# Optimization experiments

Measured on AMD Instinct MI355X. Metric: run time of the kernel, lower is better.

## Reference

```python
import jax, jax.numpy as jnp
import numpy as np

E = 1024   # embed_dim
H = 16     # num_heads
D = E // H # head_dim = 64
HD2 = D // 2
B = 2
S = 2048


def setup_inputs() -> dict:
    key = jax.random.key(0)
    ks = jax.random.split(key, 12)
    def lin(k, fan_in, fan_out):
        # xavier-uniform-ish init, stored in [in, out] (jax) convention
        lim = float(np.sqrt(6.0 / (fan_in + fan_out)))
        return jax.random.uniform(k, (fan_in, fan_out), jnp.float32, -lim, lim)
    return {
        "query": jax.random.normal(ks[0], (B, S, E), jnp.float32),
        "xi_scale": jax.random.uniform(ks[1], (B,), jnp.float32),
        "Wq": lin(ks[2], E, E), "bq": jnp.zeros((E,), jnp.float32),
        "Wk": lin(ks[3], E, E), "bk": jnp.zeros((E,), jnp.float32),
        "Wv": lin(ks[4], E, E), "bv": jnp.zeros((E,), jnp.float32),
        "Wo": lin(ks[5], E, E), "bo": jnp.zeros((E,), jnp.float32),
        "enc_w1": lin(ks[6], 1, HD2), "enc_b1": jnp.zeros((HD2,), jnp.float32),
        "ln_g": jnp.ones((HD2,), jnp.float32), "ln_b": jnp.zeros((HD2,), jnp.float32),
        "enc_w2": lin(ks[7], HD2, D), "enc_b2": jnp.zeros((D,), jnp.float32),
        "scale_gating": jnp.ones((H,), jnp.float32),
    }


def reference(query, xi_scale, Wq, bq, Wk, bk, Wv, bv, Wo, bo,
              enc_w1, enc_b1, ln_g, ln_b, enc_w2, enc_b2, scale_gating):
    b, s, e = query.shape
    h, d = H, e // H
    # --- scale adaptation: xi -> Linear -> LayerNorm -> GELU -> Linear ---
    x = xi_scale[:, None] @ enc_w1 + enc_b1                  # [B, D/2]
    mu = x.mean(-1, keepdims=True)
    var = ((x - mu) ** 2).mean(-1, keepdims=True)
    x = (x - mu) / jnp.sqrt(var + 1e-5) * ln_g + ln_b
    x = jax.nn.gelu(x, approximate=False)
    xe = x @ enc_w2 + enc_b2                                 # [B, D]
    adapt = 1.0 + jax.nn.sigmoid(scale_gating)[None, :, None] * xe[:, None, :]  # [B, H, D]
    # --- projections (self-attention: key = value = query) ---
    q = (query @ Wq + bq).reshape(b, s, h, d).transpose(0, 2, 1, 3) * adapt[:, :, None, :]
    k = (query @ Wk + bk).reshape(b, s, h, d).transpose(0, 2, 1, 3) * adapt[:, :, None, :]
    v = (query @ Wv + bv).reshape(b, s, h, d).transpose(0, 2, 1, 3)
    # --- explicit QK^T / sqrt(d) -> softmax -> V ---
    inv_scale = 1.0 / float(np.sqrt(d))
    scores = jnp.einsum('bhqd,bhkd->bhqk', q, k) * inv_scale  # [B, H, S, S]
    attn = jax.nn.softmax(scores, axis=-1)
    out = jnp.einsum('bhqk,bhkd->bhqd', attn, v)              # [B, H, S, D]
    out = out.transpose(0, 2, 1, 3).reshape(b, s, e)
    return out @ Wo + bo
```

## Files before the change

### kernel.cpp

```cpp
#include <hip/hip_runtime.h>

typedef __bf16 bf16;
typedef __attribute__((ext_vector_type(8))) __bf16 bf16x8;
typedef __attribute__((ext_vector_type(4))) float f32x4;
typedef __attribute__((ext_vector_type(16))) float f32x16;
typedef unsigned int u32;

#define MFMA16(a, b, c) __builtin_amdgcn_mfma_f32_16x16x32_bf16((a), (b), (c), 0, 0, 0)
#define MFMA32(a, b, c) __builtin_amdgcn_mfma_f32_32x32x16_bf16((a), (b), (c), 0, 0, 0)

#define BB 2
#define SS 2048
#define EE 1024
#define HH 16
#define DD 64
#define MM (BB * SS)

__device__ inline f32x4 zero4() {
    f32x4 z; z.x = 0.f; z.y = 0.f; z.z = 0.f; z.w = 0.f; return z;
}

__device__ __forceinline__ void gload16(const bf16* g, bf16* l) {
    __builtin_amdgcn_global_load_lds(
        (const __attribute__((address_space(1))) u32*)(const void*)g,
        (__attribute__((address_space(3))) u32*)(void*)l,
        16, 0, 0);
}

__device__ __forceinline__ u32 pkbf(float a, float b) {
    union { __bf16 h; unsigned short s; } ua, ub;
    ua.h = (__bf16)a; ub.h = (__bf16)b;
    return (u32)ua.s | ((u32)ub.s << 16);
}

__global__ __launch_bounds__(256) void prep_kernel(
    const float* __restrict__ query, bf16* __restrict__ qc,
    const float* __restrict__ s0, const float* __restrict__ s1,
    const float* __restrict__ s2, const float* __restrict__ s3,
    bf16* __restrict__ d0, bf16* __restrict__ d1,
    bf16* __restrict__ d2, bf16* __restrict__ d3,
    const float* __restrict__ xi, const float* __restrict__ w1,
    const float* __restrict__ b1, const float* __restrict__ lng,
    const float* __restrict__ lnb, const float* __restrict__ w2,
    const float* __restrict__ b2, const float* __restrict__ gate,
    float* __restrict__ adapt) {
    __shared__ bf16 tile[64 * 72];
    const int bid = blockIdx.x;
    const int t = threadIdx.x;

    if (bid < 2048) {
        const int i = (bid * 256 + t) * 8;
        float4 a = *(const float4*)(query + i);
        float4 b = *(const float4*)(query + i + 4);
        bf16 tmp[8];
        tmp[0] = (bf16)a.x; tmp[1] = (bf16)a.y; tmp[2] = (bf16)a.z; tmp[3] = (bf16)a.w;
        tmp[4] = (bf16)b.x; tmp[5] = (bf16)b.y; tmp[6] = (bf16)b.z; tmp[7] = (bf16)b.w;
        *(uint4*)(qc + i) = *(uint4*)tmp;
    } else if (bid < 3072) {
        const int m = (bid - 2048) >> 8;
        const int idx0 = (bid - 2048) & 255;
        const float* W = (m == 0) ? s0 : (m == 1) ? s1 : (m == 2) ? s2 : s3;
        bf16* Wt = (m == 0) ? d0 : (m == 1) ? d1 : (m == 2) ? d2 : d3;
        const int k0 = (idx0 >> 4) * 64, n0 = (idx0 & 15) * 64;
#pragma unroll
        for (int i = 0; i < 2; ++i) {
            int idx = i * 256 + t;
            int r = idx >> 3, c = (idx & 7) * 8;
            float4 a = *(const float4*)(W + (k0 + r) * EE + n0 + c);
            float4 b = *(const float4*)(W + (k0 + r) * EE + n0 + c + 4);
            bf16 tmp[8];
            tmp[0] = (bf16)a.x; tmp[1] = (bf16)a.y; tmp[2] = (bf16)a.z; tmp[3] = (bf16)a.w;
            tmp[4] = (bf16)b.x; tmp[5] = (bf16)b.y; tmp[6] = (bf16)b.z; tmp[7] = (bf16)b.w;
            *(uint4*)(tile + r * 72 + c) = *(uint4*)tmp;
        }
        __syncthreads();
#pragma unroll
        for (int i = 0; i < 2; ++i) {
            int idx = i * 256 + t;
            int n = idx >> 3, kc = (idx & 7) * 8;
            bf16 tmp[8];
#pragma unroll
            for (int j = 0; j < 8; ++j) tmp[j] = tile[(kc + j) * 72 + n];
            *(uint4*)(Wt + (n0 + n) * EE + k0 + kc) = *(uint4*)tmp;
        }
    } else {
        const int b = bid - 3072;
        float* xs = (float*)tile;
        if (t < 64) {
            const float xiv = xi[b];
            float xv = 0.f;
            if (t < 32) xv = xiv * w1[t] + b1[t];
            float sm = xv;
            for (int off = 1; off < 32; off <<= 1) sm += __shfl_xor(sm, off);
            const float mu = sm * (1.f / 32.f);
            float dv = (t < 32) ? (xv - mu) : 0.f;
            float s2 = dv * dv;
            for (int off = 1; off < 32; off <<= 1) s2 += __shfl_xor(s2, off);
            const float var = s2 * (1.f / 32.f);
            if (t < 32) {
                float xn = (xv - mu) * rsqrtf(var + 1e-5f) * lng[t] + lnb[t];
                float ge = 0.5f * xn * (1.f + erff(xn * 0.70710678118654752f));
                xs[t] = ge;
            }
        }
        __syncthreads();
        if (t < 64) {
            float acc = b2[t];
            for (int j = 0; j < 32; ++j) acc += xs[j] * w2[j * DD + t];
            for (int h = 0; h < HH; ++h) {
                float sg = 1.f / (1.f + __expf(-gate[h]));
                adapt[(b * HH + h) * DD + t] = 1.f + sg * acc;
            }
        }
    }
}

__global__ __launch_bounds__(256, 3) void gemm_qkv(
    const bf16* __restrict__ Aq, const bf16* __restrict__ Bqk,
    const bf16* __restrict__ Av,
    const float* __restrict__ bias, const float* __restrict__ bias2,
    const float* __restrict__ bias3, const float* __restrict__ adapt,
    bf16* __restrict__ outqk, bf16* __restrict__ outvt) {
    __shared__ bf16 As[2 * 128 * 32];
    __shared__ bf16 Bs[2 * 128 * 32];

    const int t = threadIdx.x;
    const int w = t >> 6, lane = t & 63;
    const int mrow = lane & 15, quad = lane >> 4;
    const int wm = (w & 1) * 64, wn = (w >> 1) * 64;

    int md, bx, by;
    const bf16 *Ap, *Bp;
    int bid = blockIdx.x;
    if (bid < 512) { md = 5; bx = bid & 31; by = bid >> 5; Ap = Aq; Bp = Bqk; }
    else { md = 4; bid -= 512; bx = bid & 7; by = bid >> 3; Ap = Av; Bp = Aq; }
    const int m0 = bx * 128, n0 = by * 128;

    f32x4 acc[4][4];
#pragma unroll
    for (int i = 0; i < 4; ++i)
#pragma unroll
        for (int j = 0; j < 4; ++j) acc[i][j] = zero4();

    const int dr = lane >> 2;
    const int dcg = ((lane & 3) ^ (dr & 3)) * 8;
    const bf16* Ag = Ap + (size_t)(m0 + w * 16 + dr) * EE + dcg;
    const bf16* Bg = Bp + (size_t)(n0 + w * 16 + dr) * EE + dcg;
    bf16* Al = As + (w * 16) * 32;
    bf16* Bl = Bs + (w * 16) * 32;

    gload16(Ag, Al);
    gload16(Ag + 64 * EE, Al + 64 * 32);
    gload16(Bg, Bl);
    gload16(Bg + 64 * EE, Bl + 64 * 32);

    for (int kt = 0; kt < 32; ++kt) {
        __syncthreads();
        if (kt < 31) {
            const int kn = (kt + 1) * 32;
            const int nb = (kt + 1) & 1;
            gload16(Ag + kn, Al + nb * 4096);
            gload16(Ag + 64 * EE + kn, Al + nb * 4096 + 64 * 32);
            gload16(Bg + kn, Bl + nb * 4096);
            gload16(Bg + 64 * EE + kn, Bl + nb * 4096 + 64 * 32);
        }
        const bf16* Ab = As + (kt & 1) * 4096;
        const bf16* Bb = Bs + (kt & 1) * 4096;
        const int sw = (quad ^ (mrow & 3)) * 8;
        bf16x8 af[4], bfr[4];
#pragma unroll
        for (int i = 0; i < 4; ++i)
            af[i] = *(const bf16x8*)(Ab + (wm + i * 16 + mrow) * 32 + sw);
#pragma unroll
        for (int j = 0; j < 4; ++j)
            bfr[j] = *(const bf16x8*)(Bb + (wn + j * 16 + mrow) * 32 + sw);
#pragma unroll
        for (int i = 0; i < 4; ++i)
#pragma unroll
            for (int j = 0; j < 4; ++j)
                acc[i][j] = MFMA16(af[i], bfr[j], acc[i][j]);
    }

#pragma unroll
    for (int i = 0; i < 4; ++i) {
#pragma unroll
        for (int j = 0; j < 4; ++j) {
            const int col = n0 + wn + j * 16 + mrow;
#pragma unroll
            for (int r = 0; r < 4; ++r) {
                const int row = m0 + wm + i * 16 + quad * 4 + r;
                float v = acc[i][j][r];
                if (md == 4) {
                    v += bias3[row];
                    const int h = row >> 6, d = row & 63;
                    const int b = col >> 11, s = col & (SS - 1);
                    outvt[(((b * HH + h) * DD + d) * SS) + s] = (bf16)v;
                } else {
                    const int m2 = col >> 10;
                    const int cl = col & 1023;
                    const int h = cl >> 6, d = cl & 63;
                    const int b = row >> 11, s = row & (SS - 1);
                    v += (m2 ? bias2[cl] : bias[cl]);
                    v *= adapt[(b * HH + h) * DD + d];
                    if (!m2) v *= 0.18033688011113811f;
                    outqk[(size_t)m2 * MM * EE + ((b * HH + h) * SS + s) * DD + d] = (bf16)v;
                }
            }
        }
    }
}

__global__ __launch_bounds__(256, 3) void gemm_o(
    const bf16* __restrict__ A, const bf16* __restrict__ Bt,
    const float* __restrict__ bias, float* __restrict__ outf) {
    __shared__ bf16 As[2 * 128 * 64];
    __shared__ bf16 Bs[2 * 64 * 64];

    const int t = threadIdx.x;
    const int w = t >> 6, lane = t & 63;
    const int mrow = lane & 15, quad = lane >> 4;
    const int m0 = blockIdx.x * 128, n0 = blockIdx.y * 64;

    f32x4 acc[2][4];
#pragma unroll
    for (int i = 0; i < 2; ++i)
#pragma unroll
        for (int j = 0; j < 4; ++j) acc[i][j] = zero4();

    const int grow = lane >> 3;
    const int gsw = ((lane & 7) ^ grow) * 8;
    const bf16* Ag = A + (size_t)(m0 + w * 32 + grow) * EE + gsw;
    const bf16* Bg = Bt + (size_t)(n0 + w * 16 + grow) * EE + gsw;
    bf16* Al = As + (w * 32) * 64;
    bf16* Bl = Bs + (w * 16) * 64;

#pragma unroll
    for (int i = 0; i < 4; ++i) gload16(Ag + i * 8 * EE, Al + i * 8 * 64);
#pragma unroll
    for (int i = 0; i < 2; ++i) gload16(Bg + i * 8 * EE, Bl + i * 8 * 64);

    for (int kt = 0; kt < 16; ++kt) {
        __syncthreads();
        if (kt < 15) {
            const int kn = (kt + 1) * 64;
            const int nb = (kt + 1) & 1;
#pragma unroll
            for (int i = 0; i < 4; ++i)
                gload16(Ag + i * 8 * EE + kn, Al + nb * 8192 + i * 8 * 64);
#pragma unroll
            for (int i = 0; i < 2; ++i)
                gload16(Bg + i * 8 * EE + kn, Bl + nb * 4096 + i * 8 * 64);
        }
        const bf16* Ab = As + (kt & 1) * 8192;
        const bf16* Bb = Bs + (kt & 1) * 4096;
#pragma unroll
        for (int ks = 0; ks < 2; ++ks) {
            const int cg = ks * 4 + quad;
            const int sw = (cg ^ (mrow & 7)) * 8;
            bf16x8 af[2], bfr[4];
#pragma unroll
            for (int mi = 0; mi < 2; ++mi)
                af[mi] = *(const bf16x8*)(Ab + (w * 32 + mi * 16 + mrow) * 64 + sw);
#pragma unroll
            for (int nj = 0; nj < 4; ++nj)
                bfr[nj] = *(const bf16x8*)(Bb + (nj * 16 + mrow) * 64 + sw);
#pragma unroll
            for (int mi = 0; mi < 2; ++mi)
#pragma unroll
                for (int nj = 0; nj < 4; ++nj)
                    acc[mi][nj] = MFMA16(af[mi], bfr[nj], acc[mi][nj]);
        }
    }

#pragma unroll
    for (int mi = 0; mi < 2; ++mi) {
#pragma unroll
        for (int nj = 0; nj < 4; ++nj) {
            const int col = n0 + nj * 16 + mrow;
#pragma unroll
            for (int r = 0; r < 4; ++r) {
                const int row = m0 + w * 32 + mi * 16 + quad * 4 + r;
                outf[row * EE + col] = acc[mi][nj][r] + bias[col];
            }
        }
    }
}

__global__ __launch_bounds__(256, 2) void attn_kernel(
    const bf16* __restrict__ q, const bf16* __restrict__ k,
    const bf16* __restrict__ vt, bf16* __restrict__ o0) {
    __shared__ bf16 lds[16384];
    bf16* Ks = lds;
    bf16* Vs = lds + 8192;

    const int t = threadIdx.x;
    const int w = t >> 6, lane = t & 63;
    const int q32 = lane & 31, h = lane >> 5;
    const int bh = blockIdx.x & 31;
    const int qb = blockIdx.x >> 5;
    const int qr0 = qb * 128 + w * 32;

    bf16x8 qf[4];
#pragma unroll
    for (int c = 0; c < 4; ++c)
        qf[c] = *(const bf16x8*)(q + (size_t)(bh * SS + qr0 + q32) * DD + c * 16 + h * 8);

    f32x16 oacc[2];
#pragma unroll
    for (int mf = 0; mf < 2; ++mf)
#pragma unroll
        for (int i = 0; i < 16; ++i) oacc[mf][i] = 0.f;
    float lsum = 0.f;

    const int dr = lane >> 3;
    const int dcg = ((lane & 7) ^ dr) * 8;
    const bf16* kg = k + (size_t)bh * SS * DD;
    const bf16* vg = vt + (size_t)bh * DD * SS;
    const bf16* kgl = kg + (size_t)dr * DD + dcg;
    const bf16* vgl = vg + (size_t)(w * 16 + dr) * SS + dcg;

#pragma unroll
    for (int i = 0; i < 2; ++i) {
        const int rb = w * 16 + i * 8;
        gload16(kgl + (size_t)rb * DD, Ks + rb * 64);
        gload16(vgl + (size_t)(i * 8) * SS, Vs + rb * 64);
    }

    for (int kt = 0; kt < SS / 64; ++kt) {
        __syncthreads();
        if (kt < SS / 64 - 1) {
            const int nb = (kt + 1) & 1;
#pragma unroll
            for (int i = 0; i < 2; ++i) {
                const int rb = w * 16 + i * 8;
                gload16(kgl + (size_t)((kt + 1) * 64 + rb) * DD, Ks + nb * 4096 + rb * 64);
                gload16(vgl + (size_t)(i * 8) * SS + (kt + 1) * 64, Vs + nb * 4096 + rb * 64);
            }
        }
        const bf16* Kb = Ks + (kt & 1) * 4096;
        const bf16* Vb = Vs + (kt & 1) * 4096;

        f32x16 st[2];
#pragma unroll
        for (int mf = 0; mf < 2; ++mf)
#pragma unroll
            for (int i = 0; i < 16; ++i) st[mf][i] = 0.f;
#pragma unroll
        for (int c = 0; c < 4; ++c) {
            const int sw = ((2 * c + h) ^ (q32 & 7)) * 8;
#pragma unroll
            for (int mf = 0; mf < 2; ++mf) {
                bf16x8 kf = *(const bf16x8*)(Kb + (mf * 32 + q32) * 64 + sw);
                st[mf] = MFMA32(kf, qf[c], st[mf]);
            }
        }

        u32 P32[2][8];
#pragma unroll
        for (int mf = 0; mf < 2; ++mf)
#pragma unroll
            for (int rp = 0; rp < 8; ++rp) {
                float pa = __builtin_amdgcn_exp2f(st[mf][2 * rp]);
                float pb = __builtin_amdgcn_exp2f(st[mf][2 * rp + 1]);
                lsum += pa + pb;
                P32[mf][rp] = pkbf(pa, pb);
            }

#pragma unroll
        for (int c = 0; c < 4; ++c) {
            const int mfs = c >> 1;
            const int ro = (c & 1) * 4;
            union { u32 u[4]; bf16x8 v; } pb;
            {
                u32 vA0 = P32[mfs][ro + 0], vA1 = P32[mfs][ro + 1];
                u32 vB0 = P32[mfs][ro + 2], vB1 = P32[mfs][ro + 3];
                u32 prep0 = h ? vA0 : vB0;
                u32 prep1 = h ? vA1 : vB1;
                u32 sh0 = __shfl_xor(prep0, 32);
                u32 sh1 = __shfl_xor(prep1, 32);
                pb.u[0] = h ? sh0 : vA0;
                pb.u[1] = h ? sh1 : vA1;
                pb.u[2] = h ? vB0 : sh0;
                pb.u[3] = h ? vB1 : sh1;
            }
            const int sw = ((2 * c + h) ^ (q32 & 7)) * 8;
#pragma unroll
            for (int mf = 0; mf < 2; ++mf) {
                bf16x8 vf = *(const bf16x8*)(Vb + (mf * 32 + q32) * 64 + sw);
                oacc[mf] = MFMA32(vf, pb.v, oacc[mf]);
            }
        }
    }

    lsum += __shfl_xor(lsum, 32);
    const float inv = 1.f / lsum;

    __syncthreads();
    bf16* ob = lds + w * 2112;
#pragma unroll
    for (int mf = 0; mf < 2; ++mf)
#pragma unroll
        for (int rp = 0; rp < 8; ++rp) {
            const int d = 32 * mf + 2 * (rp & 1) + 8 * (rp >> 1) + 4 * h;
            *(u32*)(ob + q32 * 66 + d) =
                pkbf(oacc[mf][2 * rp] * inv, oacc[mf][2 * rp + 1] * inv);
        }
    __syncthreads();

    const int b = bh >> 4, head = bh & 15;
    const int half = lane & 1;
    const int r = lane >> 1;
#pragma unroll
    for (int i = 0; i < 4; ++i) {
        bf16x8 val = *(const bf16x8*)(ob + r * 66 + half * 32 + i * 8);
        *(bf16x8*)(o0 + (size_t)(b * SS + qr0 + r) * EE + head * DD +
                   half * 32 + i * 8) = val;
    }
}

extern "C" void kernel_launch(void* const* d_in, const int* in_sizes, int n_in,
                              void* d_out, int out_size, void* d_ws, size_t ws_size,
                              hipStream_t stream) {
    const float* query = (const float*)d_in[0];
    const float* xi    = (const float*)d_in[1];
    const float* Wq = (const float*)d_in[2];  const float* bq = (const float*)d_in[3];
    const float* Wk = (const float*)d_in[4];  const float* bk = (const float*)d_in[5];
    const float* Wv = (const float*)d_in[6];  const float* bv = (const float*)d_in[7];
    const float* Wo = (const float*)d_in[8];  const float* bo = (const float*)d_in[9];
    const float* ew1 = (const float*)d_in[10]; const float* eb1 = (const float*)d_in[11];
    const float* lng = (const float*)d_in[12]; const float* lnb = (const float*)d_in[13];
    const float* ew2 = (const float*)d_in[14]; const float* eb2 = (const float*)d_in[15];
    const float* gate = (const float*)d_in[16];
    float* out = (float*)d_out;

    char* ws = (char*)d_ws;
    const size_t SZ = (size_t)MM * EE * sizeof(bf16);
    const size_t WSZ = (size_t)EE * EE * sizeof(bf16);

    bf16* queryc = (bf16*)(ws);
    bf16* p0     = (bf16*)(ws);
    bf16* qws    = (bf16*)(ws + SZ);
    bf16* kws    = (bf16*)(ws + 2 * SZ);
    bf16* vtws   = (bf16*)(ws + 3 * SZ);
    bf16* wqT    = (bf16*)(ws + 4 * SZ);
    bf16* wkT    = (bf16*)(ws + 4 * SZ + WSZ);
    bf16* wvT    = (bf16*)(ws + 4 * SZ + 2 * WSZ);
    bf16* woT    = (bf16*)(ws + 4 * SZ + 3 * WSZ);
    float* adaptws = (float*)(ws + 4 * SZ + 4 * WSZ);

    prep_kernel<<<3074, 256, 0, stream>>>(query, queryc, Wq, Wk, Wv, Wo,
                                          wqT, wkT, wvT, woT,
                                          xi, ew1, eb1, lng, lnb, ew2, eb2, gate,
                                          adaptws);

    gemm_qkv<<<768, 256, 0, stream>>>(queryc, wqT, wvT, bq, bk, bv, adaptws,
                                      qws, vtws);

    attn_kernel<<<512, 256, 0, stream>>>(qws, kws, vtws, p0);

    gemm_o<<<dim3(MM / 128, EE / 64), 256, 0, stream>>>(p0, woT, bo, out);
}
```

Baseline: 217.1 us.

## Store K and V in MFMA fragment order and load attention operands directly from global

The QKV projection epilogue now writes K and V^T in a pre-swizzled layout that matches the per-lane MFMA fragment order. The attention kernel drops the LDS double-buffered staging and its per-tile barriers, loading K and V fragments straight from global or L2 into registers, with K prefetched one tile ahead and MFMA sections given raised wave priority. This removes LDS traffic and synchronisation but leaves each wave exposed to global load latency, raises register pressure, and has every wave re-read the same K/V from cache.

```diff
diff --git a/kernel.cpp b/kernel.cpp
--- a/kernel.cpp
+++ b/kernel.cpp
@@ -194,7 +194,12 @@
                     v += bias3[row];
                     const int h = row >> 6, d = row & 63;
                     const int b = col >> 11, s = col & (SS - 1);
-                    outvt[(((b * HH + h) * DD + d) * SS) + s] = (bf16)v;
+                    const int bh = b * HH + h;
+                    const int kt2 = s >> 6, ci = (s >> 4) & 3, ji = s & 7;
+                    const int mfi = (d >> 5) & 1;
+                    const int lanei = (d & 31) + ((s >> 3) & 1) * 32;
+                    outvt[(size_t)bh * 131072 + kt2 * 4096 + mfi * 2048 +
+                          ci * 512 + lanei * 8 + ji] = (bf16)v;
                 } else {
                     const int m2 = col >> 10;
                     const int cl = col & 1023;
@@ -202,8 +207,17 @@
                     const int b = row >> 11, s = row & (SS - 1);
                     v += (m2 ? bias2[cl] : bias[cl]);
                     v *= adapt[(b * HH + h) * DD + d];
-                    if (!m2) v *= 0.18033688011113811f;
-                    outqk[(size_t)m2 * MM * EE + ((b * HH + h) * SS + s) * DD + d] = (bf16)v;
+                    if (!m2) {
+                        v *= 0.18033688011113811f;
+                        outqk[((b * HH + h) * SS + s) * DD + d] = (bf16)v;
+                    } else {
+                        const int bh = b * HH + h;
+                        const int kt2 = s >> 6, mfi = (s >> 5) & 1;
+                        const int ci = d >> 4, ji = d & 7;
+                        const int lanei = (s & 31) + ((d >> 3) & 1) * 32;
+                        outqk[(size_t)MM * EE + (size_t)bh * 131072 + kt2 * 4096 +
+                              mfi * 2048 + ci * 512 + lanei * 8 + ji] = (bf16)v;
+                    }
                 }
             }
         }
@@ -286,12 +300,77 @@
     }
 }
 
+__device__ __forceinline__ void attn_step(
+    int kt, const bf16* kbase, const bf16* vbase,
+    const bf16x8 (&qf)[4], bf16x8 (&KU)[8], bf16x8 (&KP)[8],
+    f32x16 (&oacc)[2], float (&ls)[4], int h) {
+    bf16x8 vf[8];
+#pragma unroll
+    for (int mf = 0; mf < 2; ++mf)
+#pragma unroll
+        for (int c = 0; c < 4; ++c)
+            vf[mf * 4 + c] = *(const bf16x8*)(vbase + kt * 4096 + mf * 2048 + c * 512);
+
+    f32x16 st[2];
+#pragma unroll
+    for (int mf = 0; mf < 2; ++mf)
+#pragma unroll
+        for (int i = 0; i < 16; ++i) st[mf][i] = 0.f;
+    __builtin_amdgcn_s_setprio(1);
+#pragma unroll
+    for (int c = 0; c < 4; ++c)
+#pragma unroll
+        for (int mf = 0; mf < 2; ++mf)
+            st[mf] = MFMA32(KU[mf * 4 + c], qf[c], st[mf]);
+    __builtin_amdgcn_s_setprio(0);
+
+    const int ktp = kt + (kt < SS / 64 - 1 ? 1 : 0);
+#pragma unroll
+    for (int mf = 0; mf < 2; ++mf)
+#pragma unroll
+        for (int c = 0; c < 4; ++c)
+            KP[mf * 4 + c] = *(const bf16x8*)(kbase + ktp * 4096 + mf * 2048 + c * 512);
+
+    u32 P32[2][8];
+#pragma unroll
+    for (int mf = 0; mf < 2; ++mf)
+#pragma unroll
+        for (int rp = 0; rp < 8; ++rp) {
+            float pa = __builtin_amdgcn_exp2f(st[mf][2 * rp]);
+            float pb = __builtin_amdgcn_exp2f(st[mf][2 * rp + 1]);
+            ls[rp & 3] += pa + pb;
+            P32[mf][rp] = pkbf(pa, pb);
+        }
+
+#pragma unroll
+    for (int c = 0; c < 4; ++c) {
+        const int mfs = c >> 1;
+        const int ro = (c & 1) * 4;
+        union { u32 u[4]; bf16x8 v; } pb;
+        {
+            u32 vA0 = P32[mfs][ro + 0], vA1 = P32[mfs][ro + 1];
+            u32 vB0 = P32[mfs][ro + 2], vB1 = P32[mfs][ro + 3];
+            u32 prep0 = h ? vA0 : vB0;
+            u32 prep1 = h ? vA1 : vB1;
+            u32 sh0 = __shfl_xor(prep0, 32);
+            u32 sh1 = __shfl_xor(prep1, 32);
+            pb.u[0] = h ? sh0 : vA0;
+            pb.u[1] = h ? sh1 : vA1;
+            pb.u[2] = h ? vB0 : sh0;
+            pb.u[3] = h ? vB1 : sh1;
+        }
+        __builtin_amdgcn_s_setprio(1);
+#pragma unroll
+        for (int mf = 0; mf < 2; ++mf)
+            oacc[mf] = MFMA32(vf[mf * 4 + c], pb.v, oacc[mf]);
+        __builtin_amdgcn_s_setprio(0);
+    }
+}
+
 __global__ __launch_bounds__(256, 2) void attn_kernel(
     const bf16* __restrict__ q, const bf16* __restrict__ k,
     const bf16* __restrict__ vt, bf16* __restrict__ o0) {
-    __shared__ bf16 lds[16384];
-    bf16* Ks = lds;
-    bf16* Vs = lds + 8192;
+    __shared__ bf16 lds[4 * 2112];
 
     const int t = threadIdx.x;
     const int w = t >> 6, lane = t & 63;
@@ -305,97 +384,32 @@
     for (int c = 0; c < 4; ++c)
         qf[c] = *(const bf16x8*)(q + (size_t)(bh * SS + qr0 + q32) * DD + c * 16 + h * 8);
 
+    const bf16* kbase = k + (size_t)bh * 131072 + lane * 8;
+    const bf16* vbase = vt + (size_t)bh * 131072 + lane * 8;
+
     f32x16 oacc[2];
 #pragma unroll
     for (int mf = 0; mf < 2; ++mf)
 #pragma unroll
         for (int i = 0; i < 16; ++i) oacc[mf][i] = 0.f;
-    float lsum = 0.f;
-
-    const int dr = lane >> 3;
-    const int dcg = ((lane & 7) ^ dr) * 8;
-    const bf16* kg = k + (size_t)bh * SS * DD;
-    const bf16* vg = vt + (size_t)bh * DD * SS;
-    const bf16* kgl = kg + (size_t)dr * DD + dcg;
-    const bf16* vgl = vg + (size_t)(w * 16 + dr) * SS + dcg;
-
-#pragma unroll
-    for (int i = 0; i < 2; ++i) {
-        const int rb = w * 16 + i * 8;
-        gload16(kgl + (size_t)rb * DD, Ks + rb * 64);
-        gload16(vgl + (size_t)(i * 8) * SS, Vs + rb * 64);
-    }
-
-    for (int kt = 0; kt < SS / 64; ++kt) {
-        __syncthreads();
-        if (kt < SS / 64 - 1) {
-            const int nb = (kt + 1) & 1;
-#pragma unroll
-            for (int i = 0; i < 2; ++i) {
-                const int rb = w * 16 + i * 8;
-                gload16(kgl + (size_t)((kt + 1) * 64 + rb) * DD, Ks + nb * 4096 + rb * 64);
-                gload16(vgl + (size_t)(i * 8) * SS + (kt + 1) * 64, Vs + nb * 4096 + rb * 64);
-            }
-        }
-        const bf16* Kb = Ks + (kt & 1) * 4096;
-        const bf16* Vb = Vs + (kt & 1) * 4096;
-
-        f32x16 st[2];
-#pragma unroll
-        for (int mf = 0; mf < 2; ++mf)
-#pragma unroll
-            for (int i = 0; i < 16; ++i) st[mf][i] = 0.f;
-#pragma unroll
-        for (int c = 0; c < 4; ++c) {
-            const int sw = ((2 * c + h) ^ (q32 & 7)) * 8;
-#pragma unroll
-            for (int mf = 0; mf < 2; ++mf) {
-                bf16x8 kf = *(const bf16x8*)(Kb + (mf * 32 + q32) * 64 + sw);
-                st[mf] = MFMA32(kf, qf[c], st[mf]);
-            }
-        }
-
-        u32 P32[2][8];
-#pragma unroll
-        for (int mf = 0; mf < 2; ++mf)
-#pragma unroll
-            for (int rp = 0; rp < 8; ++rp) {
-                float pa = __builtin_amdgcn_exp2f(st[mf][2 * rp]);
-                float pb = __builtin_amdgcn_exp2f(st[mf][2 * rp + 1]);
-                lsum += pa + pb;
-                P32[mf][rp] = pkbf(pa, pb);
-            }
-
-#pragma unroll
-        for (int c = 0; c < 4; ++c) {
-            const int mfs = c >> 1;
-            const int ro = (c & 1) * 4;
-            union { u32 u[4]; bf16x8 v; } pb;
-            {
-                u32 vA0 = P32[mfs][ro + 0], vA1 = P32[mfs][ro + 1];
-                u32 vB0 = P32[mfs][ro + 2], vB1 = P32[mfs][ro + 3];
-                u32 prep0 = h ? vA0 : vB0;
-                u32 prep1 = h ? vA1 : vB1;
-                u32 sh0 = __shfl_xor(prep0, 32);
-                u32 sh1 = __shfl_xor(prep1, 32);
-                pb.u[0] = h ? sh0 : vA0;
-                pb.u[1] = h ? sh1 : vA1;
-                pb.u[2] = h ? vB0 : sh0;
-                pb.u[3] = h ? vB1 : sh1;
-            }
-            const int sw = ((2 * c + h) ^ (q32 & 7)) * 8;
-#pragma unroll
-            for (int mf = 0; mf < 2; ++mf) {
-                bf16x8 vf = *(const bf16x8*)(Vb + (mf * 32 + q32) * 64 + sw);
-                oacc[mf] = MFMA32(vf, pb.v, oacc[mf]);
-            }
-        }
-    }
-
+    float ls[4] = {0.f, 0.f, 0.f, 0.f};
+
+    bf16x8 Ka[8], Kb[8];
+#pragma unroll
+    for (int mf = 0; mf < 2; ++mf)
+#pragma unroll
+        for (int c = 0; c < 4; ++c)
+            Ka[mf * 4 + c] = *(const bf16x8*)(kbase + mf * 2048 + c * 512);
+
+    for (int kt2 = 0; kt2 < SS / 128; ++kt2) {
+        attn_step(2 * kt2,     kbase, vbase, qf, Ka, Kb, oacc, ls, h);
+        attn_step(2 * kt2 + 1, kbase, vbase, qf, Kb, Ka, oacc, ls, h);
+    }
+
+    float lsum = (ls[0] + ls[1]) + (ls[2] + ls[3]);
     lsum += __shfl_xor(lsum, 32);
     const float inv = 1.f / lsum;
 
-    __syncthreads();
     bf16* ob = lds + w * 2112;
 #pragma unroll
     for (int mf = 0; mf < 2; ++mf)
```

Result: no change. 215.7 us (-0.6%).
